# Optimization experiments

Measured on AMD Instinct MI355X. Metric: run time of the kernel, lower is better.

The kernel has to match this reference:

```python
import jax, jax.numpy as jnp
import numpy as np


def setup_inputs() -> dict:
    key = jax.random.key(0)
    B, C, A, P, N = 4, 1, 180, 384, 256
    sinogram = jax.random.normal(key, (B, C, A, P), dtype=jnp.float32)
    # projection angles uniformly covering [0, pi)
    thetas = jnp.linspace(0.0, np.pi, A, endpoint=False).astype(jnp.float32)
    # uniformly spaced detector positions centered at 0, unit spacing
    positions = jnp.arange(P, dtype=jnp.float32) - (P - 1) / 2.0
    return {"sinogram": sinogram, "thetas": thetas, "positions": positions, "image_size": N}


def reference(sinogram, thetas, positions, image_size):
    """Radon backprojection: image[y,x] = sum_a interp(sinogram[a], x*cos+y*sin)."""
    B, C, A, P = sinogram.shape
    N = image_size
    # pixel-center coordinates, image centered at origin (y axis pointing up)
    c = jnp.arange(N, dtype=sinogram.dtype) - (N - 1) / 2.0
    xs = c[None, :]          # [1, N]
    ys = -c[:, None]         # [N, 1]
    cos = jnp.cos(thetas)[:, None, None]  # [A, 1, 1]
    sin = jnp.sin(thetas)[:, None, None]
    t = xs[None] * cos + ys[None] * sin   # [A, N, N] detector coordinate per (angle, pixel)
    # fractional index into the (uniform) detector position grid
    dp = positions[1] - positions[0]
    f = (t - positions[0]) / dp           # [A, N, N]
    i0 = jnp.floor(f)
    w = f - i0                            # linear interpolation weight
    valid = (i0 >= 0) & (i0 <= P - 2)     # rays falling inside the detector
    i0c = jnp.clip(i0, 0, P - 2).astype(jnp.int32)
    idx = i0c.reshape(A, N * N)[None, None]          # [1, 1, A, N*N]
    v0 = jnp.take_along_axis(sinogram, idx, axis=3)  # [B, C, A, N*N]
    v1 = jnp.take_along_axis(sinogram, idx + 1, axis=3)
    wf = w.reshape(A, N * N)[None, None]
    vm = valid.reshape(A, N * N)[None, None]
    val = jnp.where(vm, v0 * (1.0 - wf) + v1 * wf, 0.0)
    return val.sum(axis=2).reshape(B, C, N, N)
```

## Files before the change

kernel.cpp:

```cpp
#include <hip/hip_runtime.h>
#include <cmath>


template <int BATCH>
__global__ __launch_bounds__(256) void radon_bwd_kernel(
    const float* __restrict__ sino,
    const float* __restrict__ thetas,
    const float* __restrict__ positions,
    float* __restrict__ out,
    int A, int P, int N, int chunk)
{
    __shared__ float s_cs[256];
    __shared__ float s_sn[256];
    const int tid = threadIdx.x;
    if (tid < A) {
        float th = thetas[tid];
        s_cs[tid] = cosf(th);
        s_sn[tid] = sinf(th);
    }
    __syncthreads();

    const int nn  = N * N;
    const int pix = blockIdx.x * blockDim.x + tid;
    if (pix >= nn) return;

    const int a0 = blockIdx.y * chunk;
    const int a1 = min(A, a0 + chunk);

    const int x = pix % N;
    const int y = pix / N;
    const float half = (float)(N - 1) * 0.5f;
    const float cx = (float)x - half;
    const float cy = half - (float)y;

    const float p0     = positions[0];
    const float inv_dp = 1.0f / (positions[1] - p0);

    const int bstride = A * P;

    float acc[BATCH];
#pragma unroll
    for (int b = 0; b < BATCH; ++b) acc[b] = 0.0f;

    for (int a = a0; a < a1; ++a) {
        float f   = fmaf(cx, s_cs[a], fmaf(cy, s_sn[a], -p0)) * inv_dp;
        float i0f = floorf(f);
        int   i0  = (int)i0f;
        float w   = f - i0f;
        if (i0 >= 0 && i0 <= P - 2) {
            const float* row = sino + a * P + i0;
#pragma unroll
            for (int b = 0; b < BATCH; ++b) {
                float v0 = row[(size_t)b * bstride];
                float v1 = row[(size_t)b * bstride + 1];
                acc[b] = fmaf(w, v1 - v0, acc[b] + v0);
            }
        }
    }

    float* ob = out + pix;
#pragma unroll
    for (int b = 0; b < BATCH; ++b)
        atomicAdd(ob + (size_t)b * nn, acc[b]);
}

extern "C" void kernel_launch(void* const* d_in, const int* in_sizes, int n_in,
                              void* d_out, int out_size, void* d_ws, size_t ws_size,
                              hipStream_t stream) {
    const float* sino      = (const float*)d_in[0];
    const float* thetas    = (const float*)d_in[1];
    const float* positions = (const float*)d_in[2];
    float* out             = (float*)d_out;

    const int A  = in_sizes[1];
    const int P  = in_sizes[2];
    const int BC = in_sizes[0] / (A * P);
    const int N  = (int)lroundf(sqrtf((float)(out_size / BC)));
    const int nn = N * N;

    hipMemsetAsync(d_out, 0, (size_t)out_size * sizeof(float), stream);

    const int ACHUNKS = 8;
    const int chunk   = (A + ACHUNKS - 1) / ACHUNKS;

    dim3 block(256);
    if (BC == 4 && A <= 256) {
        dim3 grid((nn + 255) / 256, ACHUNKS);
        radon_bwd_kernel<4><<<grid, block, 0, stream>>>(
            sino, thetas, positions, out, A, P, N, chunk);
    } else {
        dim3 grid((nn + 255) / 256, 1);
        for (int b = 0; b < BC; ++b) {
            radon_bwd_kernel<1><<<grid, block, 0, stream>>>(
                sino + (size_t)b * A * P, thetas, positions,
                out + (size_t)b * nn, A, P, N, A);
        }
    }
}
```

Before: 86.87 us.

## Replace atomic accumulation with per-chunk partial buffers and a reduction kernel

Each angle-chunk block writes its per-pixel sums to a workspace slice instead of atomically adding into a zeroed output. A second kernel sums the slices. This removes the memset and the atomics. The detector spacing scale is also folded into the cached cos/sin table, saving a multiply per angle. In exchange it adds several MB of workspace traffic and an extra launch. The fallback path, used when the workspace is too small, is a much slower single-pass kernel.

```diff
diff --git a/kernel.cpp b/kernel.cpp
--- a/kernel.cpp
+++ b/kernel.cpp
@@ -3,20 +3,22 @@
 
 
 template <int BATCH>
-__global__ __launch_bounds__(256) void radon_bwd_kernel(
+__global__ __launch_bounds__(256) void radon_partial_kernel(
     const float* __restrict__ sino,
     const float* __restrict__ thetas,
     const float* __restrict__ positions,
-    float* __restrict__ out,
+    float* __restrict__ part,
     int A, int P, int N, int chunk)
 {
     __shared__ float s_cs[256];
     __shared__ float s_sn[256];
     const int tid = threadIdx.x;
+    const float p0     = positions[0];
+    const float inv_dp = 1.0f / (positions[1] - p0);
     if (tid < A) {
         float th = thetas[tid];
-        s_cs[tid] = cosf(th);
-        s_sn[tid] = sinf(th);
+        s_cs[tid] = cosf(th) * inv_dp;
+        s_sn[tid] = sinf(th) * inv_dp;
     }
     __syncthreads();
 
@@ -32,9 +34,7 @@
     const float half = (float)(N - 1) * 0.5f;
     const float cx = (float)x - half;
     const float cy = half - (float)y;
-
-    const float p0     = positions[0];
-    const float inv_dp = 1.0f / (positions[1] - p0);
+    const float q0 = -p0 * inv_dp;
 
     const int bstride = A * P;
 
@@ -43,7 +43,7 @@
     for (int b = 0; b < BATCH; ++b) acc[b] = 0.0f;
 
     for (int a = a0; a < a1; ++a) {
-        float f   = fmaf(cx, s_cs[a], fmaf(cy, s_sn[a], -p0)) * inv_dp;
+        float f   = fmaf(cx, s_cs[a], fmaf(cy, s_sn[a], q0));
         float i0f = floorf(f);
         int   i0  = (int)i0f;
         float w   = f - i0f;
@@ -58,10 +58,56 @@
         }
     }
 
-    float* ob = out + pix;
+    float* pp = part + ((size_t)blockIdx.y * BATCH) * nn + pix;
 #pragma unroll
-    for (int b = 0; b < BATCH; ++b)
-        atomicAdd(ob + (size_t)b * nn, acc[b]);
+    for (int b = 0; b < BATCH; ++b) pp[(size_t)b * nn] = acc[b];
+}
+
+__global__ __launch_bounds__(256) void radon_reduce_kernel(
+    const float* __restrict__ part,
+    float* __restrict__ out,
+    int BN, int nchunks)
+{
+    int i = blockIdx.x * blockDim.x + threadIdx.x;
+    if (i >= BN) return;
+    float s = 0.0f;
+    for (int c = 0; c < nchunks; ++c)
+        s += part[(size_t)c * BN + i];
+    out[i] = s;
+}
+
+__global__ __launch_bounds__(256) void radon_atomic_kernel(
+    const float* __restrict__ sino,
+    const float* __restrict__ thetas,
+    const float* __restrict__ positions,
+    float* __restrict__ out,
+    int A, int P, int N, int BC)
+{
+    const int nn  = N * N;
+    const int pix = blockIdx.x * blockDim.x + threadIdx.x;
+    if (pix >= nn) return;
+    const float p0     = positions[0];
+    const float inv_dp = 1.0f / (positions[1] - p0);
+    const int x = pix % N;
+    const int y = pix / N;
+    const float half = (float)(N - 1) * 0.5f;
+    const float cx = (float)x - half;
+    const float cy = half - (float)y;
+    for (int b = 0; b < BC; ++b) {
+        float acc = 0.0f;
+        for (int a = 0; a < A; ++a) {
+            float th = thetas[a];
+            float f  = (cx * cosf(th) + cy * sinf(th) - p0) * inv_dp;
+            float i0f = floorf(f);
+            int i0 = (int)i0f;
+            float w = f - i0f;
+            if (i0 >= 0 && i0 <= P - 2) {
+                const float* row = sino + ((size_t)b * A + a) * P + i0;
+                acc = fmaf(w, row[1] - row[0], acc + row[0]);
+            }
+        }
+        out[(size_t)b * nn + pix] = acc;
+    }
 }
 
 extern "C" void kernel_launch(void* const* d_in, const int* in_sizes, int n_in,
@@ -78,22 +124,23 @@
     const int N  = (int)lroundf(sqrtf((float)(out_size / BC)));
     const int nn = N * N;
 
-    hipMemsetAsync(d_out, 0, (size_t)out_size * sizeof(float), stream);
-
     const int ACHUNKS = 8;
     const int chunk   = (A + ACHUNKS - 1) / ACHUNKS;
+    const size_t need = (size_t)ACHUNKS * BC * nn * sizeof(float);
 
-    dim3 block(256);
-    if (BC == 4 && A <= 256) {
-        dim3 grid((nn + 255) / 256, ACHUNKS);
-        radon_bwd_kernel<4><<<grid, block, 0, stream>>>(
-            sino, thetas, positions, out, A, P, N, chunk);
+    if (BC == 4 && A <= 256 && ws_size >= need) {
+        float* part = (float*)d_ws;
+        dim3 block(256);
+        dim3 grid1((nn + 255) / 256, ACHUNKS);
+        radon_partial_kernel<4><<<grid1, block, 0, stream>>>(
+            sino, thetas, positions, part, A, P, N, chunk);
+        const int BN = BC * nn;
+        dim3 grid2((BN + 255) / 256);
+        radon_reduce_kernel<<<grid2, block, 0, stream>>>(part, out, BN, ACHUNKS);
     } else {
-        dim3 grid((nn + 255) / 256, 1);
-        for (int b = 0; b < BC; ++b) {
-            radon_bwd_kernel<1><<<grid, block, 0, stream>>>(
-                sino + (size_t)b * A * P, thetas, positions,
-                out + (size_t)b * nn, A, P, N, A);
-        }
+        dim3 block(256);
+        dim3 grid((nn + 255) / 256);
+        radon_atomic_kernel<<<grid, block, 0, stream>>>(
+            sino, thetas, positions, out, A, P, N, BC);
     }
 }
```

Result: no change. 88.33 us (+1.7%).
